# Kernel tuning notes

Hardware: AMD Instinct MI355X
Metric: run time of the kernel (lower is better)

The kernel has to match this reference:

```python
import jax, jax.numpy as jnp
from jax import lax
import numpy as np

NEG = -1.0e9


def setup_inputs() -> dict:
    key = jax.random.key(0)
    k1, k2, k3 = jax.random.split(key, 3)
    B, N, W = 512, 8192, 15
    token_scores = jax.random.normal(k1, (B, N), dtype=jnp.float32)
    attention_mask = jax.random.randint(k2, (B, N), 0, 2).astype(jnp.int32)
    gamma = jnp.float32(1.0)
    width_logits = 0.1 * jax.random.normal(k3, (W,), dtype=jnp.float32)
    return {
        "token_scores": token_scores,
        "attention_mask": attention_mask,
        "gamma": gamma,
        "width_logits": width_logits,
    }


def _span_boost(masked, width_weights, max_span_width):
    # masked: [B, N] scores with padding set to NEG
    B, N = masked.shape
    boost = jnp.full((B, N), NEG, dtype=masked.dtype)
    for w in range(2, min(max_span_width + 1, N + 1)):
        # sliding min over windows of size w -> [B, N-w+1] (one per window start)
        span_mins = lax.reduce_window(
            masked, jnp.inf, lax.min,
            window_dimensions=(1, w), window_strides=(1, 1), padding="VALID")
        weighted = span_mins * width_weights[w - 2]
        # token p gets max over all window starts s with s <= p <= s+w-1:
        # sliding max with left/right pad (w-1) maps [B,N-w+1] back to [B,N]
        tok_boost = lax.reduce_window(
            weighted, -jnp.inf, lax.max,
            window_dimensions=(1, w), window_strides=(1, 1),
            padding=((0, 0), (w - 1, w - 1)))
        boost = jnp.maximum(boost, tok_boost)
    return boost


def reference(token_scores, attention_mask, gamma, width_logits):
    max_span_width = width_logits.shape[0]
    masked = jnp.where(attention_mask == 0, jnp.float32(NEG), token_scores)
    width_weights = jax.nn.softmax(width_logits, axis=0)
    boost = _span_boost(masked, width_weights, max_span_width)
    boost = jnp.maximum(boost, masked)
    return token_scores + gamma * boost
```

## Files before the change

### kernel.cpp

```cpp
#include <hip/hip_runtime.h>
#include <math.h>


constexpr float NEGV = -1.0e9f;
constexpr int W = 15;
constexpr int HALO = 16;
constexpr int TPT = 4;
constexpr int BLK = 256;
constexpr int TOKS = BLK * TPT;
constexpr int TILE_F = TOKS + 2 * HALO;
constexpr int TILE_F4 = TILE_F / 4;

__global__ __launch_bounds__(BLK)
void span_boost_kernel(const float* __restrict__ scores,
                       const int* __restrict__ mask,
                       const float* __restrict__ gamma_p,
                       const float* __restrict__ wlogits,
                       float* __restrict__ out,
                       int N, int chunksPerRow) {
    __shared__ __align__(16) float tile[TILE_F];
    __shared__ float wwS[W];

    const int tid = threadIdx.x;
    const int blk = blockIdx.x;
    const int row = blk / chunksPerRow;
    const int c0 = (blk - row * chunksPerRow) * TOKS;
    const size_t rowOff = (size_t)row * (size_t)N;
    const float4* s4row = (const float4*)(scores + rowOff);
    const int4*   m4row = (const int4*)(mask + rowOff);

    if (tid == 0) {
        float m = wlogits[0];
        #pragma unroll
        for (int i = 1; i < W; ++i) m = fmaxf(m, wlogits[i]);
        float e[W]; float s = 0.f;
        #pragma unroll
        for (int i = 0; i < W; ++i) { e[i] = expf(wlogits[i] - m); s += e[i]; }
        const float inv = 1.0f / s;
        #pragma unroll
        for (int i = 0; i < W; ++i) wwS[i] = e[i] * inv;
    }

    const int g4base = c0 / 4 - HALO / 4;
    const int n4 = N / 4;
    #pragma unroll
    for (int l = tid; l < TILE_F4; l += BLK) {
        const int g4 = g4base + l;
        float4 v = make_float4(-INFINITY, -INFINITY, -INFINITY, -INFINITY);
        if (g4 >= 0 && g4 < n4) {
            const float4 sc = s4row[g4];
            const int4   mk = m4row[g4];
            v.x = (mk.x == 0) ? NEGV : sc.x;
            v.y = (mk.y == 0) ? NEGV : sc.y;
            v.z = (mk.z == 0) ? NEGV : sc.z;
            v.w = (mk.w == 0) ? NEGV : sc.w;
        }
        ((float4*)tile)[l] = v;
    }

    __syncthreads();

    float ww[W - 1];
    #pragma unroll
    for (int i = 0; i < W - 1; ++i)
        ww[i] = __int_as_float(__builtin_amdgcn_readfirstlane(__float_as_int(wwS[i])));

    const int fb = tid * TPT;
    float w[36];
    #pragma unroll
    for (int q = 0; q < 9; ++q) {
        const float4 v = *(const float4*)&tile[fb + 4 * q];
        w[4 * q + 0] = v.x; w[4 * q + 1] = v.y; w[4 * q + 2] = v.z; w[4 * q + 3] = v.w;
    }

    const int gp4 = c0 / 4 + tid;
    const float4 sc4 = s4row[gp4];
    const float myScore[TPT] = { sc4.x, sc4.y, sc4.z, sc4.w };
    const float gamma = gamma_p[0];

    float res[TPT];
    #pragma unroll
    for (int r = 0; r < TPT; ++r) {
        const float vp = w[16 + r];
        float Ap[W], Bp[W];
        Ap[0] = vp; Bp[0] = vp;
        #pragma unroll
        for (int j = 1; j < W; ++j) Ap[j] = fminf(Ap[j - 1], w[16 + r - j]);
        #pragma unroll
        for (int k = 1; k < W; ++k) Bp[k] = fminf(Bp[k - 1], w[16 + r + k]);

        float boost = -INFINITY;
        #pragma unroll
        for (int t = 1; t <= W - 1; ++t) {
            float d = fmaxf(Ap[t], Bp[t]);
            #pragma unroll
            for (int j = 1; j < t; ++j)
                d = fmaxf(d, fminf(Ap[j], Bp[t - j]));
            boost = fmaxf(boost, d * ww[t - 1]);
        }
        res[r] = myScore[r] + gamma * fmaxf(boost, vp);
    }

    float4 o4 = make_float4(res[0], res[1], res[2], res[3]);
    ((float4*)(out + rowOff))[gp4] = o4;
}

extern "C" void kernel_launch(void* const* d_in, const int* in_sizes, int n_in,
                              void* d_out, int out_size, void* d_ws, size_t ws_size,
                              hipStream_t stream) {
    const float* scores = (const float*)d_in[0];
    const int*   maskp  = (const int*)d_in[1];
    const float* gammap = (const float*)d_in[2];
    const float* wl     = (const float*)d_in[3];
    float* outp = (float*)d_out;

    const int N = 8192;
    const int B = in_sizes[0] / N;
    const int chunksPerRow = N / TOKS;
    dim3 grid(B * chunksPerRow);
    span_boost_kernel<<<grid, BLK, 0, stream>>>(scores, maskp, gammap, wl, outp,
                                                N, chunksPerRow);
}
```

Baseline: 106.9 us.

## Replace quadratic span min-max scan with bitonic merge of prefix minima

Each window width previously had its own max-over-splits of min(prefix, suffix), which costs O(W^2) min/max operations per token. The new code builds a 16-element bitonic sequence from the left and right running minima. A 4-stage bitonic merge sorts it in descending order, so the t-th element gives the best span minimum for width t+1, and the weighted max needs only one pass. This cuts ALU work in what looks like a compute-bound kernel, but it relies on the order-statistic identity being exact, including the boundary entries and the NEG/-inf padding.

```diff
diff --git a/kernel.cpp b/kernel.cpp
--- a/kernel.cpp
+++ b/kernel.cpp
@@ -81,23 +81,37 @@
     float res[TPT];
     #pragma unroll
     for (int r = 0; r < TPT; ++r) {
-        const float vp = w[16 + r];
+        const int c = 16 + r;
+        const float vp = w[c];
         float Ap[W], Bp[W];
         Ap[0] = vp; Bp[0] = vp;
         #pragma unroll
-        for (int j = 1; j < W; ++j) Ap[j] = fminf(Ap[j - 1], w[16 + r - j]);
+        for (int j = 1; j < W; ++j) {
+            Ap[j] = fminf(Ap[j - 1], w[c - j]);
+            Bp[j] = fminf(Bp[j - 1], w[c + j]);
+        }
+
+        float s[16];
+        s[0] = Ap[1]; s[1] = Ap[2];
         #pragma unroll
-        for (int k = 1; k < W; ++k) Bp[k] = fminf(Bp[k - 1], w[16 + r + k]);
+        for (int i = 2; i <= 13; ++i) s[i] = fmaxf(Ap[i + 1], Bp[16 - i]);
+        s[14] = Bp[2]; s[15] = Bp[1];
 
-        float boost = -INFINITY;
         #pragma unroll
-        for (int t = 1; t <= W - 1; ++t) {
-            float d = fmaxf(Ap[t], Bp[t]);
+        for (int d = 8; d >= 1; d >>= 1) {
             #pragma unroll
-            for (int j = 1; j < t; ++j)
-                d = fmaxf(d, fminf(Ap[j], Bp[t - j]));
-            boost = fmaxf(boost, d * ww[t - 1]);
+            for (int i = 0; i < 16; ++i) {
+                if (!(i & d)) {
+                    const float a = s[i], b = s[i | d];
+                    s[i] = fmaxf(a, b);
+                    s[i | d] = fminf(a, b);
+                }
+            }
         }
+        float boost = ww[0] * s[0];
+        #pragma unroll
+        for (int i = 1; i < 14; ++i) boost = fmaxf(boost, ww[i] * s[i]);
+
         res[r] = myScore[r] + gamma * fmaxf(boost, vp);
     }
 
```

Measured after the change: 98.80 us. 1.08x faster.
